# Kernel tuning notes

Measured on AMD Instinct MI355X. Metric: run time of the kernel, lower is better.

## Reference

```python
import jax, jax.numpy as jnp
import numpy as np

B, S, D = 2, 2048, 2048
H, HKV = 32, 8
HD = D // H  # 64
NEG_INF = -1e9


def _rope_tables(seq_len, head_dim):
    inv_freq = 1.0 / (10000.0 ** (np.arange(0, head_dim, 2, dtype=np.float32) / head_dim))
    t = np.arange(seq_len, dtype=np.float32)
    freqs = np.outer(t, inv_freq)                      # (S, HD/2)
    emb = np.concatenate([freqs, freqs], axis=-1)      # (S, HD)
    cos = np.cos(emb)[None, None]                      # (1,1,S,HD)
    sin = np.sin(emb)[None, None]
    return jnp.asarray(cos), jnp.asarray(sin)


def setup_inputs() -> dict:
    key = jax.random.key(0)
    ks = jax.random.split(key, 5)
    hidden_states = jax.random.normal(ks[0], (B, S, D), dtype=jnp.float32)
    # causal additive mask: 0 where allowed, -inf (large negative) where masked
    causal = jnp.tril(jnp.ones((S, S), dtype=jnp.bool_))
    attention_mask = jnp.where(causal, 0.0, NEG_INF).astype(jnp.float32)
    attention_mask = jnp.broadcast_to(attention_mask[None, None], (B, 1, S, S))
    cos, sin = _rope_tables(S, HD)
    sc = 0.02
    Wq = jax.random.normal(ks[1], (D, H * HD), dtype=jnp.float32) * sc
    Wk = jax.random.normal(ks[2], (D, HKV * HD), dtype=jnp.float32) * sc
    Wv = jax.random.normal(ks[3], (D, HKV * HD), dtype=jnp.float32) * sc
    Wo = jax.random.normal(ks[4], (H * HD, D), dtype=jnp.float32) * sc
    return {"hidden_states": hidden_states, "attention_mask": attention_mask,
            "cos": cos, "sin": sin, "Wq": Wq, "Wk": Wk, "Wv": Wv, "Wo": Wo}


def _rotate_half(x):
    x1, x2 = jnp.split(x, 2, axis=-1)
    return jnp.concatenate([-x2, x1], axis=-1)


def _apply_rope(x, cos, sin):
    # x: (B, h, S, HD); cos/sin: (1,1,S,HD)
    return x * cos + _rotate_half(x) * sin


def reference(hidden_states, attention_mask, cos, sin, Wq, Wk, Wv, Wo):
    b, s, _ = hidden_states.shape
    scale = 1.0 / np.sqrt(HD)
    q = (hidden_states @ Wq).reshape(b, s, H, HD).transpose(0, 2, 1, 3)    # (B,H,S,HD)
    k = (hidden_states @ Wk).reshape(b, s, HKV, HD).transpose(0, 2, 1, 3)  # (B,HKV,S,HD)
    v = (hidden_states @ Wv).reshape(b, s, HKV, HD).transpose(0, 2, 1, 3)
    q = _apply_rope(q, cos, sin)
    k = _apply_rope(k, cos, sin)
    # GQA: group query heads per kv head without materializing repeated KV
    g = H // HKV
    qg = q.reshape(b, HKV, g, s, HD)
    scores = jnp.einsum('bkgqd,bksd->bkgqs', qg, k) * scale               # (B,HKV,g,S,S)
    scores = scores + attention_mask[:, :, None]                          # broadcast (B,1,1,S,S)
    attn = jax.nn.softmax(scores, axis=-1)
    out = jnp.einsum('bkgqs,bksd->bkgqd', attn, v)                        # (B,HKV,g,S,HD)
    out = out.reshape(b, H, s, HD).transpose(0, 2, 1, 3).reshape(b, s, H * HD)
    return out @ Wo
```

## Files before the change

kernel.cpp:

```cpp
#include <hip/hip_runtime.h>
#include <math.h>

typedef _Float16 half8 __attribute__((ext_vector_type(8)));
typedef _Float16 half4 __attribute__((ext_vector_type(4)));
typedef _Float16 half2 __attribute__((ext_vector_type(2)));
typedef float f32x4 __attribute__((ext_vector_type(4)));

#define S_LEN 2048
#define DM    2048
#define NH    32
#define NKV   8

#define QSCALE 0.1803368801111204f
#define NSHIFT -11.541560327111707f

#if __has_builtin(__builtin_amdgcn_exp2f)
#define EXP2(x) __builtin_amdgcn_exp2f(x)
#else
#define EXP2(x) __builtin_exp2f(x)
#endif

__device__ __forceinline__ half2 pkrtz(float a, float b) {
    return __builtin_bit_cast(half2, __builtin_amdgcn_cvt_pkrtz(a, b));
}

__device__ __forceinline__ void async16(const void* g, void* l) {
    __builtin_amdgcn_global_load_lds(
        (const __attribute__((address_space(1))) unsigned int*)g,
        (__attribute__((address_space(3))) unsigned int*)l, 16, 0, 0);
}

__global__ __launch_bounds__(256) void prep_all(
    const float* __restrict__ Wq, const float* __restrict__ Wk,
    const float* __restrict__ Wv, const float* __restrict__ Wo,
    const float* __restrict__ hidden,
    _Float16* __restrict__ Wqkv_t, _Float16* __restrict__ Wo_t,
    _Float16* __restrict__ hid_h)
{
    const int z = blockIdx.z;
    if (z == 4) {
        const size_t i = ((size_t)(blockIdx.y * 64 + blockIdx.x) * 256 + threadIdx.x) * 8;
        float4 v0 = *(const float4*)(hidden + i);
        float4 v1 = *(const float4*)(hidden + i + 4);
        half8 o = {(_Float16)v0.x, (_Float16)v0.y, (_Float16)v0.z, (_Float16)v0.w,
                   (_Float16)v1.x, (_Float16)v1.y, (_Float16)v1.z, (_Float16)v1.w};
        *(half8*)(hid_h + i) = o;
        return;
    }
    const float* W; _Float16* Wt; int N;
    if (z == 0)      { W = Wq; Wt = Wqkv_t;                        N = 2048; }
    else if (z == 1) { W = Wk; Wt = Wqkv_t + (size_t)2048 * 2048;  N = 512;  }
    else if (z == 2) { W = Wv; Wt = Wqkv_t + (size_t)2560 * 2048;  N = 512;  }
    else             { W = Wo; Wt = Wo_t;                          N = 2048; }
    if ((int)blockIdx.x * 32 >= N) return;

    __shared__ float t[32][33];
    const int n0 = blockIdx.x * 32, k0 = blockIdx.y * 32;
    const int tx = threadIdx.x & 31, ty = threadIdx.x >> 5;
#pragma unroll
    for (int i = 0; i < 32; i += 8)
        t[ty + i][tx] = W[(size_t)(k0 + ty + i) * N + n0 + tx];
    __syncthreads();
#pragma unroll
    for (int i = 0; i < 32; i += 8)
        Wt[(size_t)(n0 + ty + i) * 2048 + k0 + tx] = (_Float16)t[tx][ty + i];
}

__global__ __launch_bounds__(512, 2) void gemm_h(
    const _Float16* __restrict__ A, const _Float16* __restrict__ Bt,
    void* __restrict__ Cout, int N, int K, int mode,
    const float* __restrict__ cosT, const float* __restrict__ sinT)
{
    __shared__ __align__(16) _Float16 Lds[2][4][8192];
    const int tid  = threadIdx.x;
    const int lane = tid & 63;
    const int wave = tid >> 6;
    const int lm = lane & 15, quad = lane >> 4;
    const int wm = wave >> 2;
    const int wn = wave & 3;

    const int gx  = gridDim.x;
    const int nwg = gx * gridDim.y;
    const int lin = blockIdx.y * gx + blockIdx.x;
    const int tsw = (lin & 7) * (nwg >> 3) + (lin >> 3);
    const int bm  = (tsw / gx) * 256, bn = (tsw % gx) * 256;
    const int nt  = K >> 6;

    const int sr   = tid >> 3;
    const int lg   = (tid & 7) ^ (sr & 7);
    const int grow = sr * 2 + (lg >> 2);
    const int gcol = (lg & 3) << 3;
    const _Float16* pA0 = A  + (size_t)(bm + grow) * K + gcol;
    const _Float16* pB0 = Bt + (size_t)(bn + grow) * K + gcol;
    char* ldsb = (char*)Lds + tid * 16;

#define STAGE(t, idx) do { if ((t) < nt) {                          \
        const int koff_ = (t) * 64 + (((idx) >> 1) << 5);           \
        const _Float16* s_ = (((idx) & 1) ? pA0 : pB0) + koff_;     \
        char* d_ = ldsb + (((t) & 1) << 16) + ((idx) << 14);        \
        async16(s_, d_);                                            \
        async16(s_ + (size_t)128 * K, d_ + 8192);                   \
    } } while (0)

    const int chsw = (((((lm & 1) << 2) | quad) ^ (lm >> 1)) << 3);
    const int ar = (wm << 6) + (lm >> 1);
    const int br = (wn << 5) + (lm >> 1);
    const _Float16* Lh = (const _Float16*)Lds;

    f32x4 acc[8][4];
#pragma unroll
    for (int i = 0; i < 8; ++i)
#pragma unroll
        for (int j = 0; j < 4; ++j) acc[i][j] = (f32x4){0.f, 0.f, 0.f, 0.f};

    STAGE(0, 0); STAGE(0, 1); STAGE(0, 2); STAGE(0, 3);
    if (nt > 1) asm volatile("s_waitcnt vmcnt(4)" ::: "memory");
    else        asm volatile("s_waitcnt vmcnt(0)" ::: "memory");
    __builtin_amdgcn_s_barrier();

    half8 af[8], bf[4];
#define MFMA32()                                                              \
    _Pragma("unroll") for (int i_ = 0; i_ < 8; ++i_)                          \
    _Pragma("unroll") for (int j_ = 0; j_ < 4; ++j_)                          \
        acc[i_][j_] = __builtin_amdgcn_mfma_f32_16x16x32_f16(                 \
            af[i_], bf[j_], acc[i_][j_], 0, 0, 0);

#define PH_TAIL(cond)                                                         \
    __builtin_amdgcn_s_setprio(0);                                            \
    if (cond) asm volatile("s_waitcnt vmcnt(4)" ::: "memory");                \
    else      asm volatile("s_waitcnt vmcnt(0)" ::: "memory");                \
    __builtin_amdgcn_s_barrier()

    int p = 0;
    for (int G = 0; G < nt; ++G, p ^= 1) {
        const _Float16* Lp = Lh + (p << 15);
        const _Float16* Au0 = Lp + 8192  + ar * 64 + chsw;
        const _Float16* Au1 = Lp + 24576 + ar * 64 + chsw;
        const _Float16* Bu0 = Lp +         br * 64 + chsw;
        const _Float16* Bu1 = Lp + 16384 + br * 64 + chsw;
        const bool more = (G + 1) < nt;
#pragma unroll
        for (int i = 0; i < 8; ++i) af[i] = *(const half8*)(Au0 + i * 512);
#pragma unroll
        for (int j = 0; j < 4; ++j) bf[j] = *(const half8*)(Bu0 + j * 512);
        STAGE(G + 1, 0); STAGE(G + 1, 1);
        __builtin_amdgcn_s_setprio(1);
        MFMA32();
        PH_TAIL(more);
#pragma unroll
        for (int i = 0; i < 8; ++i) af[i] = *(const half8*)(Au1 + i * 512);
#pragma unroll
        for (int j = 0; j < 4; ++j) bf[j] = *(const half8*)(Bu1 + j * 512);
        STAGE(G + 1, 2); STAGE(G + 1, 3);
        __builtin_amdgcn_s_setprio(1);
        MFMA32();
        PH_TAIL(more);
    }
#undef STAGE
#undef MFMA32
#undef PH_TAIL

    const int mrowq = bm + (wm << 7) + (quad << 2);
    if (mode == 0) {
        float* C = (float*)Cout;
        const int col0 = bn + (wn << 6) + lm;
#pragma unroll
        for (int mf = 0; mf < 8; ++mf)
#pragma unroll
            for (int r = 0; r < 4; ++r) {
                const int m = mrowq + mf * 16 + r;
#pragma unroll
                for (int nf = 0; nf < 4; ++nf)
                    C[(size_t)m * N + col0 + nf * 16] = acc[mf][nf][r];
            }
        return;
    }

    _Float16* Cq = (_Float16*)Cout;
    _Float16* Ck = Cq + (size_t)2 * NH * S_LEN * 64;
    _Float16* Cv = Ck + (size_t)2 * NKV * S_LEN * 64;
    const int colbase = bn + (wn << 6);
    const int region = (colbase >= 2560) ? 2 : (colbase >= 2048) ? 1 : 0;

    if (region == 2) {
        const int head = (colbase - 2560) >> 6;
#pragma unroll
        for (int mf = 0; mf < 8; ++mf) {
            const int m0 = mrowq + mf * 16;
            const int b = m0 >> 11, s0 = m0 & 2047;
#pragma unroll
            for (int nf = 0; nf < 4; ++nf) {
                half2 lo = pkrtz(acc[mf][nf][0], acc[mf][nf][1]);
                half2 hi = pkrtz(acc[mf][nf][2], acc[mf][nf][3]);
                half4 ov = {lo[0], lo[1], hi[0], hi[1]};
                *(half4*)(Cv + ((((size_t)b * NKV + head) << 6) + lm + nf * 16) * S_LEN + s0) = ov;
            }
        }
        return;
    }

    const float qscale = (region == 0) ? QSCALE : 1.0f;
    const int head = (region == 0) ? (colbase >> 6) : ((colbase - 2048) >> 6);
    _Float16* Cdst = (region == 0) ? Cq : Ck;
    const int nh = (region == 0) ? NH : NKV;
#pragma unroll
    for (int mf = 0; mf < 8; ++mf)
#pragma unroll
        for (int r = 0; r < 4; ++r) {
            int m = mrowq + mf * 16 + r;
            int b = m >> 11, s = m & 2047;
            const float c0 = cosT[s * 64 + lm], c16 = cosT[s * 64 + lm + 16];
            const float s0 = sinT[s * 64 + lm], s16 = sinT[s * 64 + lm + 16];
            float a0r = acc[mf][0][r], a1r = acc[mf][1][r];
            float a2r = acc[mf][2][r], a3r = acc[mf][3][r];
            float o0 = (a0r * c0  - a2r * s0)  * qscale;
            float o1 = (a1r * c16 - a3r * s16) * qscale;
            float o2 = (a2r * c0  + a0r * s0)  * qscale;
            float o3 = (a3r * c16 + a1r * s16) * qscale;
            _Float16* d = Cdst + ((((size_t)b * nh + head) * S_LEN + s) << 6) + lm;
            d[0]  = (_Float16)o0;
            d[16] = (_Float16)o1;
            d[32] = (_Float16)o2;
            d[48] = (_Float16)o3;
        }
}

#define LSWOFS(row, halfofs) \
    ((row) * 64 + (((((halfofs) >> 3) & 7) ^ ((row) & 7)) << 3) + ((halfofs) & 7))

__global__ __launch_bounds__(256, 2) void attn_h(
    const _Float16* __restrict__ q, const _Float16* __restrict__ k,
    const _Float16* __restrict__ vt, _Float16* __restrict__ x2)
{
    __shared__ __align__(16) _Float16 Ks[2][64 * 64];
    __shared__ __align__(16) _Float16 Vts[2][64 * 64];

    const int kvh = blockIdx.y, b = blockIdx.z;
    const int tid = threadIdx.x;
    const int wave = tid >> 6, lane = tid & 63;
    const int lm = lane & 15, quad = lane >> 4;
    const int h = kvh * 4 + wave;

    const int qtT[2] = {63 - (int)blockIdx.x, (int)blockIdx.x};
    const int ktm[2] = {(qtT[0] * 32 + 31) >> 6, (qtT[1] * 32 + 31) >> 6};

    const _Float16* kbase  = k  + ((((size_t)b * NKV + kvh) * S_LEN) << 6);
    const _Float16* vtbase = vt + ((((size_t)b * NKV + kvh) << 6) * S_LEN);

    half8 qf[2][2][2];
#pragma unroll
    for (int tp = 0; tp < 2; ++tp) {
        const _Float16* qb = q + ((((size_t)b * NH + h) * S_LEN + qtT[tp] * 32) << 6);
#pragma unroll
        for (int i = 0; i < 2; ++i)
#pragma unroll
            for (int kk = 0; kk < 2; ++kk)
                qf[tp][i][kk] = *(const half8*)(qb + (i * 16 + lm) * 64 + kk * 32 + quad * 8);
    }

    f32x4 accOT[2][2][4];
    float lpart[2][2];
#pragma unroll
    for (int tp = 0; tp < 2; ++tp)
#pragma unroll
        for (int i = 0; i < 2; ++i) {
            lpart[tp][i] = 0.f;
#pragma unroll
            for (int j = 0; j < 4; ++j) accOT[tp][i][j] = (f32x4){0.f, 0.f, 0.f, 0.f};
        }

    const int f0 = tid * 16, f1 = 4096 + tid * 16;
    const int r0 = f0 >> 7, r1 = f1 >> 7;
    const int c0 = ((f0 >> 4) & 7) ^ (r0 & 7);
    const int c1 = ((f1 >> 4) & 7) ^ (r1 & 7);
    const char* ksrc0 = (const char*)kbase  + r0 * 128 + c0 * 16;
    const char* ksrc1 = (const char*)kbase  + r1 * 128 + c1 * 16;
    const char* vsrc0 = (const char*)vtbase + (size_t)r0 * 4096 + c0 * 16;
    const char* vsrc1 = (const char*)vtbase + (size_t)r1 * 4096 + c1 * 16;

#define STAGEKV(kt, nb) do {                                          \
        async16(ksrc0 + (size_t)(kt) * 8192, (char*)Ks[nb]  + f0);    \
        async16(ksrc1 + (size_t)(kt) * 8192, (char*)Ks[nb]  + f1);    \
        async16(vsrc0 + (kt) * 128,          (char*)Vts[nb] + f0);    \
        async16(vsrc1 + (kt) * 128,          (char*)Vts[nb] + f1);    \
    } while (0)

    STAGEKV(0, 0);
    asm volatile("s_waitcnt vmcnt(0)" ::: "memory");
    __builtin_amdgcn_s_barrier();

    for (int kt = 0; kt <= ktm[0]; ++kt) {
        const int cur = kt & 1;
        if (kt < ktm[0]) STAGEKV(kt + 1, cur ^ 1);
        const _Float16* Kc = Ks[cur];
        const _Float16* Vc = Vts[cur];

        half8 kf[4][2];
        half4 vtf[4][4];
#pragma unroll
        for (int t = 0; t < 4; ++t) {
#pragma unroll
            for (int kk = 0; kk < 2; ++kk)
                kf[t][kk] = *(const half8*)(Kc + LSWOFS(t * 16 + lm, kk * 32 + quad * 8));
#pragma unroll
            for (int j = 0; j < 4; ++j)
                vtf[j][t] = *(const half4*)(Vc + LSWOFS(j * 16 + lm, t * 16 + quad * 4));
        }

#pragma unroll
        for (int tp = 0; tp < 2; ++tp) {
            if (kt > ktm[tp]) continue;
            const bool diag = (kt == ktm[tp]);
#pragma unroll
            for (int i = 0; i < 2; ++i) {
                f32x4 sc[4];
                __builtin_amdgcn_s_setprio(1);
#pragma unroll
                for (int t = 0; t < 4; ++t) {
                    f32x4 z = (f32x4){NSHIFT, NSHIFT, NSHIFT, NSHIFT};
                    z = __builtin_amdgcn_mfma_f32_16x16x32_f16(kf[t][0], qf[tp][i][0], z, 0, 0, 0);
                    z = __builtin_amdgcn_mfma_f32_16x16x32_f16(kf[t][1], qf[tp][i][1], z, 0, 0, 0);
                    sc[t] = z;
                }
                __builtin_amdgcn_s_setprio(0);
                if (diag) {
                    const int qpos = qtT[tp] * 32 + i * 16 + lm;
#pragma unroll
                    for (int t = 0; t < 4; ++t)
#pragma unroll
                        for (int r = 0; r < 4; ++r) {
                            int key = kt * 64 + t * 16 + quad * 4 + r;
                            if (key > qpos) sc[t][r] = -30000.f;
                        }
                }
                half4 pt[4];
                float lp = 0.f;
#pragma unroll
                for (int t = 0; t < 4; ++t) {
                    float p0 = EXP2(sc[t][0]), p1 = EXP2(sc[t][1]);
                    float p2 = EXP2(sc[t][2]), p3 = EXP2(sc[t][3]);
                    lp += (p0 + p1) + (p2 + p3);
                    half2 lo = pkrtz(p0, p1);
                    half2 hi = pkrtz(p2, p3);
                    pt[t] = (half4){lo[0], lo[1], hi[0], hi[1]};
                }
                lpart[tp][i] += lp;
                __builtin_amdgcn_s_setprio(1);
#pragma unroll
                for (int j = 0; j < 4; ++j)
#pragma unroll
                    for (int t = 0; t < 4; ++t)
                        accOT[tp][i][j] = __builtin_amdgcn_mfma_f32_16x16x16f16(
                            vtf[j][t], pt[t], accOT[tp][i][j], 0, 0, 0);
                __builtin_amdgcn_s_setprio(0);
            }
        }
        asm volatile("s_waitcnt vmcnt(0)" ::: "memory");
        __builtin_amdgcn_s_barrier();
    }
#undef STAGEKV

#pragma unroll
    for (int tp = 0; tp < 2; ++tp)
#pragma unroll
        for (int i = 0; i < 2; ++i) {
            float l = lpart[tp][i];
            l += __shfl_xor(l, 16);
            l += __shfl_xor(l, 32);
            const float inv = 1.f / l;
            const size_t row = (size_t)b * S_LEN + qtT[tp] * 32 + i * 16 + lm;
#pragma unroll
            for (int j = 0; j < 4; ++j) {
                f32x4 o = accOT[tp][i][j];
                half2 lo = pkrtz(o[0] * inv, o[1] * inv);
                half2 hi = pkrtz(o[2] * inv, o[3] * inv);
                half4 ov = {lo[0], lo[1], hi[0], hi[1]};
                *(half4*)(x2 + row * DM + h * 64 + j * 16 + quad * 4) = ov;
            }
        }
}

extern "C" void kernel_launch(void* const* d_in, const int* in_sizes, int n_in,
                              void* d_out, int out_size, void* d_ws, size_t ws_size,
                              hipStream_t stream)
{
    const float* hidden = (const float*)d_in[0];
    const float* cosT = (const float*)d_in[2];
    const float* sinT = (const float*)d_in[3];
    const float* Wq = (const float*)d_in[4];
    const float* Wk = (const float*)d_in[5];
    const float* Wv = (const float*)d_in[6];
    const float* Wo = (const float*)d_in[7];
    float* out = (float*)d_out;

    _Float16* w = (_Float16*)d_ws;
    _Float16* hid_h  = w;  w += (size_t)4096 * 2048;
    _Float16* Wqkv_t = w;  w += (size_t)3072 * 2048;
    _Float16* Wo_t   = w;  w += (size_t)2048 * 2048;
    _Float16* qh     = w;  w += (size_t)2 * NH * S_LEN * 64;
    _Float16* kh     = w;  w += (size_t)2 * NKV * S_LEN * 64;
    _Float16* vth    = w;  w += (size_t)2 * NKV * S_LEN * 64;
    _Float16* x2h    = w;

    dim3 blk(256);
    prep_all<<<dim3(64, 64, 5), blk, 0, stream>>>(Wq, Wk, Wv, Wo, hidden,
                                                  Wqkv_t, Wo_t, hid_h);

    gemm_h<<<dim3(12, 16), dim3(512), 0, stream>>>(hid_h, Wqkv_t, qh, 3072, 2048, 1, cosT, sinT);

    attn_h<<<dim3(32, 8, 2), blk, 0, stream>>>(qh, kh, vth, x2h);

    gemm_h<<<dim3(8, 16), dim3(512), 0, stream>>>(x2h, Wo_t, out, 2048, 2048, 0, nullptr, nullptr);
}
```

Measured before the change: 307.9 us.

## Shrink GEMM tiles to 128x128 with 256 threads and single-buffered LDS

Replaces the 256x256-tile, 512-thread double-buffered GEMM with a 128x128-tile, 256-thread kernel that uses one LDS buffer per operand and a simple wait, compute, barrier, load loop. This gives four times as many workgroups and smaller per-block LDS and register use, so more blocks can be resident and the grid fills the 256 CUs better. In exchange it drops the async prefetch overlap and the priority tricks, and data reuse per tile is lower, so the kernel moves more global traffic and loses latency hiding.

```diff
diff --git a/kernel.cpp b/kernel.cpp
--- a/kernel.cpp
+++ b/kernel.cpp
@@ -66,106 +66,87 @@
         Wt[(size_t)(n0 + ty + i) * 2048 + k0 + tx] = (_Float16)t[tx][ty + i];
 }
 
-__global__ __launch_bounds__(512, 2) void gemm_h(
+__global__ __launch_bounds__(256, 3) void gemm_h(
     const _Float16* __restrict__ A, const _Float16* __restrict__ Bt,
     void* __restrict__ Cout, int N, int K, int mode,
     const float* __restrict__ cosT, const float* __restrict__ sinT)
 {
-    __shared__ __align__(16) _Float16 Lds[2][4][8192];
+    __shared__ __align__(16) _Float16 Al[128 * 64];
+    __shared__ __align__(16) _Float16 Bl[128 * 64];
     const int tid  = threadIdx.x;
     const int lane = tid & 63;
     const int wave = tid >> 6;
     const int lm = lane & 15, quad = lane >> 4;
-    const int wm = wave >> 2;
-    const int wn = wave & 3;
+    const int wm = wave >> 1;
+    const int wn = wave & 1;
 
     const int gx  = gridDim.x;
     const int nwg = gx * gridDim.y;
     const int lin = blockIdx.y * gx + blockIdx.x;
     const int tsw = (lin & 7) * (nwg >> 3) + (lin >> 3);
-    const int bm  = (tsw / gx) * 256, bn = (tsw % gx) * 256;
+    const int bm  = (tsw / gx) * 128, bn = (tsw % gx) * 128;
     const int nt  = K >> 6;
 
-    const int sr   = tid >> 3;
-    const int lg   = (tid & 7) ^ (sr & 7);
-    const int grow = sr * 2 + (lg >> 2);
-    const int gcol = (lg & 3) << 3;
-    const _Float16* pA0 = A  + (size_t)(bm + grow) * K + gcol;
-    const _Float16* pB0 = Bt + (size_t)(bn + grow) * K + gcol;
-    char* ldsb = (char*)Lds + tid * 16;
-
-#define STAGE(t, idx) do { if ((t) < nt) {                          \
-        const int koff_ = (t) * 64 + (((idx) >> 1) << 5);           \
-        const _Float16* s_ = (((idx) & 1) ? pA0 : pB0) + koff_;     \
-        char* d_ = ldsb + (((t) & 1) << 16) + ((idx) << 14);        \
-        async16(s_, d_);                                            \
-        async16(s_ + (size_t)128 * K, d_ + 8192);                   \
-    } } while (0)
-
-    const int chsw = (((((lm & 1) << 2) | quad) ^ (lm >> 1)) << 3);
-    const int ar = (wm << 6) + (lm >> 1);
-    const int br = (wn << 5) + (lm >> 1);
-    const _Float16* Lh = (const _Float16*)Lds;
-
-    f32x4 acc[8][4];
-#pragma unroll
-    for (int i = 0; i < 8; ++i)
+    const int r8   = tid >> 3;
+    const int gcol = ((tid & 7) ^ (r8 & 7)) << 3;
+    const _Float16* pA = A  + (size_t)(bm + r8) * K + gcol;
+    const _Float16* pB = Bt + (size_t)(bn + r8) * K + gcol;
+    char* ldsA = (char*)Al + tid * 16;
+    char* ldsB = (char*)Bl + tid * 16;
+
+#define STAGE(t) do {                                                     \
+        const int ko_ = (t) * 64;                                         \
+        _Pragma("unroll")                                                 \
+        for (int u_ = 0; u_ < 4; ++u_) {                                  \
+            async16(pA + (size_t)(u_ * 32) * K + ko_, ldsA + u_ * 4096);  \
+            async16(pB + (size_t)(u_ * 32) * K + ko_, ldsB + u_ * 4096);  \
+        }                                                                 \
+    } while (0)
+
+    const int cs0 = ((quad       ^ (lm & 7)) << 3);
+    const int cs1 = (((4 + quad) ^ (lm & 7)) << 3);
+    const _Float16* Arow = Al + (wm * 64 + lm) * 64;
+    const _Float16* Brow = Bl + (wn * 64 + lm) * 64;
+
+    f32x4 acc[4][4];
+#pragma unroll
+    for (int i = 0; i < 4; ++i)
 #pragma unroll
         for (int j = 0; j < 4; ++j) acc[i][j] = (f32x4){0.f, 0.f, 0.f, 0.f};
 
-    STAGE(0, 0); STAGE(0, 1); STAGE(0, 2); STAGE(0, 3);
-    if (nt > 1) asm volatile("s_waitcnt vmcnt(4)" ::: "memory");
-    else        asm volatile("s_waitcnt vmcnt(0)" ::: "memory");
-    __builtin_amdgcn_s_barrier();
-
-    half8 af[8], bf[4];
-#define MFMA32()                                                              \
-    _Pragma("unroll") for (int i_ = 0; i_ < 8; ++i_)                          \
+#define MFMA16()                                                              \
+    _Pragma("unroll") for (int i_ = 0; i_ < 4; ++i_)                          \
     _Pragma("unroll") for (int j_ = 0; j_ < 4; ++j_)                          \
         acc[i_][j_] = __builtin_amdgcn_mfma_f32_16x16x32_f16(                 \
             af[i_], bf[j_], acc[i_][j_], 0, 0, 0);
 
-#define PH_TAIL(cond)                                                         \
-    __builtin_amdgcn_s_setprio(0);                                            \
-    if (cond) asm volatile("s_waitcnt vmcnt(4)" ::: "memory");                \
-    else      asm volatile("s_waitcnt vmcnt(0)" ::: "memory");                \
-    __builtin_amdgcn_s_barrier()
-
-    int p = 0;
-    for (int G = 0; G < nt; ++G, p ^= 1) {
-        const _Float16* Lp = Lh + (p << 15);
-        const _Float16* Au0 = Lp + 8192  + ar * 64 + chsw;
-        const _Float16* Au1 = Lp + 24576 + ar * 64 + chsw;
-        const _Float16* Bu0 = Lp +         br * 64 + chsw;
-        const _Float16* Bu1 = Lp + 16384 + br * 64 + chsw;
-        const bool more = (G + 1) < nt;
-#pragma unroll
-        for (int i = 0; i < 8; ++i) af[i] = *(const half8*)(Au0 + i * 512);
-#pragma unroll
-        for (int j = 0; j < 4; ++j) bf[j] = *(const half8*)(Bu0 + j * 512);
-        STAGE(G + 1, 0); STAGE(G + 1, 1);
-        __builtin_amdgcn_s_setprio(1);
-        MFMA32();
-        PH_TAIL(more);
-#pragma unroll
-        for (int i = 0; i < 8; ++i) af[i] = *(const half8*)(Au1 + i * 512);
-#pragma unroll
-        for (int j = 0; j < 4; ++j) bf[j] = *(const half8*)(Bu1 + j * 512);
-        STAGE(G + 1, 2); STAGE(G + 1, 3);
-        __builtin_amdgcn_s_setprio(1);
-        MFMA32();
-        PH_TAIL(more);
+    STAGE(0);
+    for (int kt = 0; kt < nt; ++kt) {
+        asm volatile("s_waitcnt vmcnt(0)" ::: "memory");
+        __builtin_amdgcn_s_barrier();
+        half8 af[4], bf[4];
+#pragma unroll
+        for (int i = 0; i < 4; ++i) af[i] = *(const half8*)(Arow + i * 1024 + cs0);
+#pragma unroll
+        for (int j = 0; j < 4; ++j) bf[j] = *(const half8*)(Brow + j * 1024 + cs0);
+        MFMA16();
+#pragma unroll
+        for (int i = 0; i < 4; ++i) af[i] = *(const half8*)(Arow + i * 1024 + cs1);
+#pragma unroll
+        for (int j = 0; j < 4; ++j) bf[j] = *(const half8*)(Brow + j * 1024 + cs1);
+        MFMA16();
+        __builtin_amdgcn_s_barrier();
+        if (kt + 1 < nt) STAGE(kt + 1);
     }
 #undef STAGE
-#undef MFMA32
-#undef PH_TAIL
-
-    const int mrowq = bm + (wm << 7) + (quad << 2);
+#undef MFMA16
+
+    const int mrowq = bm + wm * 64 + (quad << 2);
     if (mode == 0) {
         float* C = (float*)Cout;
-        const int col0 = bn + (wn << 6) + lm;
-#pragma unroll
-        for (int mf = 0; mf < 8; ++mf)
+        const int col0 = bn + wn * 64 + lm;
+#pragma unroll
+        for (int mf = 0; mf < 4; ++mf)
 #pragma unroll
             for (int r = 0; r < 4; ++r) {
                 const int m = mrowq + mf * 16 + r;
@@ -179,13 +160,13 @@
     _Float16* Cq = (_Float16*)Cout;
     _Float16* Ck = Cq + (size_t)2 * NH * S_LEN * 64;
     _Float16* Cv = Ck + (size_t)2 * NKV * S_LEN * 64;
-    const int colbase = bn + (wn << 6);
+    const int colbase = bn + wn * 64;
     const int region = (colbase >= 2560) ? 2 : (colbase >= 2048) ? 1 : 0;
 
     if (region == 2) {
         const int head = (colbase - 2560) >> 6;
 #pragma unroll
-        for (int mf = 0; mf < 8; ++mf) {
+        for (int mf = 0; mf < 4; ++mf) {
             const int m0 = mrowq + mf * 16;
             const int b = m0 >> 11, s0 = m0 & 2047;
 #pragma unroll
@@ -204,7 +185,7 @@
     _Float16* Cdst = (region == 0) ? Cq : Ck;
     const int nh = (region == 0) ? NH : NKV;
 #pragma unroll
-    for (int mf = 0; mf < 8; ++mf)
+    for (int mf = 0; mf < 4; ++mf)
 #pragma unroll
         for (int r = 0; r < 4; ++r) {
             int m = mrowq + mf * 16 + r;
@@ -406,9 +387,9 @@
     prep_all<<<dim3(64, 64, 5), blk, 0, stream>>>(Wq, Wk, Wv, Wo, hidden,
                                                   Wqkv_t, Wo_t, hid_h);
 
-    gemm_h<<<dim3(12, 16), dim3(512), 0, stream>>>(hid_h, Wqkv_t, qh, 3072, 2048, 1, cosT, sinT);
+    gemm_h<<<dim3(24, 32), blk, 0, stream>>>(hid_h, Wqkv_t, qh, 3072, 2048, 1, cosT, sinT);
 
     attn_h<<<dim3(32, 8, 2), blk, 0, stream>>>(qh, kh, vth, x2h);
 
-    gemm_h<<<dim3(8, 16), dim3(512), 0, stream>>>(x2h, Wo_t, out, 2048, 2048, 0, nullptr, nullptr);
-}
+    gemm_h<<<dim3(16, 32), blk, 0, stream>>>(x2h, Wo_t, out, 2048, 2048, 0, nullptr, nullptr);
+}
```

Result: faster. 287.5 us (-6.6%).
